# Optimization experiments

Measured on AMD Instinct MI355X. Metric: run time of the kernel, lower is better.

## Reference

```python
import jax, jax.numpy as jnp
import numpy as np

RADIUS, HMIN, HMAX, NSAMPLE = 0.05, -0.02, 0.04, 32
EPS = 1e-5


def setup_inputs() -> dict:
    key = jax.random.key(0)
    ks = jax.random.split(key, 6)
    B, N, C, OUT = 4, 2048, 256, 256
    seed_xyz_graspable = jax.random.uniform(ks[0], (B, N, 3), jnp.float32) * 0.2
    seed_features_graspable = jax.random.normal(ks[1], (B, C, N), jnp.float32)
    vp_rot = jax.random.normal(ks[2], (B, N, 3, 3), jnp.float32)
    W1 = jax.random.normal(ks[3], (OUT, 3 + C), jnp.float32) * 0.02
    W2 = jax.random.normal(ks[4], (OUT, OUT), jnp.float32) * 0.02
    return {
        "seed_xyz_graspable": seed_xyz_graspable,
        "seed_features_graspable": seed_features_graspable,
        "vp_rot": vp_rot,
        "W1": W1, "gamma1": jnp.ones((OUT,), jnp.float32), "beta1": jnp.zeros((OUT,), jnp.float32),
        "W2": W2, "gamma2": jnp.ones((OUT,), jnp.float32), "beta2": jnp.zeros((OUT,), jnp.float32),
    }


def _cylinder_query(xyz, rot):
    # xyz: (B,N,3), rot: (B,N,3,3); new_xyz == xyz.
    B, N, _ = xyz.shape
    d = xyz[:, None, :, :] - xyz[:, :, None, :]                  # (B,P,N,3) offsets to each candidate
    r = jnp.einsum('bpij,bpnj->bpni', rot, d)                    # rotate into cylinder frame (rot @ d)
    mask = (r[..., 1] ** 2 + r[..., 2] ** 2 < RADIUS ** 2) & (r[..., 0] > HMIN) & (r[..., 0] < HMAX)
    order = jnp.arange(N, dtype=jnp.int32)
    keys = jnp.where(mask, order, order + N)                     # in-cylinder points sort first, stable order
    _, idx = jax.lax.top_k(-keys, NSAMPLE)                       # first NSAMPLE indices satisfying the query
    valid = jnp.take_along_axis(mask, idx, axis=-1)
    first = idx[..., :1]
    any_valid = valid[..., :1]
    idx = jnp.where(valid, idx, jnp.where(any_valid, first, 0))  # pad with first hit like the CUDA kernel
    return idx                                                   # (B,P,NSAMPLE) int32


def _group(xyz, features, rot, idx):
    gxyz = jax.vmap(lambda a, i: a[i])(xyz, idx)                 # (B,P,S,3)
    gxyz = (gxyz - xyz[:, :, None, :]) / RADIUS                  # center on query + normalize_xyz
    gxyz = jnp.einsum('bpsj,bpjk->bpsk', gxyz, rot)              # rotate_xyz: grouped_xyz @ rot
    gfeat = jax.vmap(lambda f, i: f[:, i])(features, idx)        # (B,C,P,S)
    return jnp.concatenate([gxyz.transpose(0, 3, 1, 2), gfeat], axis=1)  # (B,3+C,P,S)


def _conv_bn_relu(x, W, gamma, beta):
    y = jnp.einsum('oc,bcps->bops', W, x)                        # 1x1 conv, no bias (bn=True)
    mu = y.mean(axis=(0, 2, 3), keepdims=True)
    var = y.var(axis=(0, 2, 3), keepdims=True)
    y = (y - mu) * jax.lax.rsqrt(var + EPS)
    y = y * gamma[None, :, None, None] + beta[None, :, None, None]
    return jax.nn.relu(y)


def reference(seed_xyz_graspable, seed_features_graspable, vp_rot, W1, gamma1, beta1, W2, gamma2, beta2):
    idx = _cylinder_query(seed_xyz_graspable, vp_rot)
    g = _group(seed_xyz_graspable, seed_features_graspable, vp_rot, idx)
    h = _conv_bn_relu(g, W1, gamma1, beta1)
    h = _conv_bn_relu(h, W2, gamma2, beta2)
    return h.max(axis=3)                                         # maxpool over nsample -> (B,OUT,P)
```

## Files before the change

kernel.cpp:

```cpp
#include <hip/hip_runtime.h>

typedef unsigned short u16;
typedef unsigned int u32;
typedef __attribute__((ext_vector_type(8))) short bf16x8;
typedef __attribute__((ext_vector_type(4))) float f32x4;

#define NPTS 2048
#define CFEAT 256
#define NS 32
#define MTOT 262144
#define NBLK 4096
#define NROW 8192
#define INV_N (1.0f/262144.0f)

__device__ __forceinline__ float bf2f(u16 u) {
    union { u32 i; float f; } v; v.i = ((u32)u) << 16; return v.f;
}
__device__ __forceinline__ u16 f2bf(float f) {
    union { float f; u32 i; } v; v.f = f;
    u32 i = v.i;
    return (u16)((i + 0x7fffu + ((i >> 16) & 1u)) >> 16);
}

__device__ __forceinline__ void gload16(const void* g, void* l) {
    __builtin_amdgcn_global_load_lds((const __attribute__((address_space(1))) void*)g,
                                     (__attribute__((address_space(3))) void*)l, 16, 0, 0);
}

__global__ __launch_bounds__(256) void prep_k(const float* __restrict__ W1, const float* __restrict__ W2,
                                              u16* __restrict__ Wp1, u16* __restrict__ Wp2) {
    int o = blockIdx.x, t = threadIdx.x;
    Wp1[o * 288 + t] = f2bf(W1[o * 259 + 3 + t]);
    if (t < 32) Wp1[o * 288 + 256 + t] = (t < 3) ? f2bf(W1[o * 259 + t]) : (u16)0;
    Wp2[o * 256 + t] = f2bf(W2[o * 256 + t]);
}

__global__ __launch_bounds__(256) void query_k(const float* __restrict__ xyz, const float* __restrict__ rot,
                                               int* __restrict__ idx) {
    int pid = blockIdx.x * 4 + (threadIdx.x >> 6);
    int lane = threadIdx.x & 63;
    int b = pid >> 11, p = pid & 2047;
    const float* xb = xyz + (size_t)b * NPTS * 3;
    float px = xb[p * 3 + 0], py = xb[p * 3 + 1], pz = xb[p * 3 + 2];
    const float* rp = rot + (size_t)pid * 9;
    float r00 = rp[0], r01 = rp[1], r02 = rp[2];
    float r10 = rp[3], r11 = rp[4], r12 = rp[5];
    float r20 = rp[6], r21 = rp[7], r22 = rp[8];
    int cnt = 0, first = 0;
    for (int n0 = 0; n0 < NPTS && cnt < NS; n0 += 64) {
        int n = n0 + lane;
        float dx = __fsub_rn(xb[n * 3 + 0], px);
        float dy = __fsub_rn(xb[n * 3 + 1], py);
        float dz = __fsub_rn(xb[n * 3 + 2], pz);
        float a0 = __fadd_rn(__fadd_rn(__fmul_rn(r00, dx), __fmul_rn(r01, dy)), __fmul_rn(r02, dz));
        float a1 = __fadd_rn(__fadd_rn(__fmul_rn(r10, dx), __fmul_rn(r11, dy)), __fmul_rn(r12, dz));
        float a2 = __fadd_rn(__fadd_rn(__fmul_rn(r20, dx), __fmul_rn(r21, dy)), __fmul_rn(r22, dz));
        float t2 = __fadd_rn(__fmul_rn(a1, a1), __fmul_rn(a2, a2));
        bool valid = (t2 < 0.0025f) && (a0 > -0.02f) && (a0 < 0.04f);
        unsigned long long bal = __ballot(valid);
        if (cnt == 0 && bal) first = n0 + __builtin_ctzll(bal);
        int rank = __builtin_popcountll(bal & ((1ull << lane) - 1ull));
        int slot = cnt + rank;
        if (valid && slot < NS) idx[(size_t)pid * NS + slot] = n;
        cnt += __builtin_popcountll(bal);
    }
    int filled = cnt < NS ? cnt : NS;
    if (lane >= filled && lane < NS) idx[(size_t)pid * NS + lane] = (cnt > 0) ? first : 0;
}

__global__ __launch_bounds__(256) void featT_k(const float* __restrict__ feat, u16* __restrict__ featT) {
    __shared__ float sm[32 * 33];
    int b = blockIdx.z;
    int n0 = blockIdx.x * 32, c0 = blockIdx.y * 32;
    int t = threadIdx.x, x = t & 31, y = t >> 5;
    #pragma unroll
    for (int rr = 0; rr < 4; rr++) {
        int c = c0 + y + rr * 8;
        sm[(y + rr * 8) * 33 + x] = feat[((size_t)(b * CFEAT + c)) * NPTS + n0 + x];
    }
    __syncthreads();
    #pragma unroll
    for (int rr = 0; rr < 4; rr++) {
        int n = n0 + y + rr * 8;
        featT[((size_t)(b * NPTS + n)) * CFEAT + c0 + x] = f2bf(sm[x * 33 + (y + rr * 8)]);
    }
}

__global__ __launch_bounds__(256) void gxyz_k(const float* __restrict__ xyz, const float* __restrict__ rot,
                                              const int* __restrict__ idx, u16* __restrict__ gxyz) {
    int m = blockIdx.x * 256 + threadIdx.x;
    int pid = m >> 5;
    int b = pid >> 11, p = pid & 2047;
    int i = idx[m];
    const float* xb = xyz + (size_t)b * NPTS * 3;
    float dx = (xb[i * 3 + 0] - xb[p * 3 + 0]) * 20.0f;
    float dy = (xb[i * 3 + 1] - xb[p * 3 + 1]) * 20.0f;
    float dz = (xb[i * 3 + 2] - xb[p * 3 + 2]) * 20.0f;
    const float* rp = rot + (size_t)pid * 9;
    float g0 = dx * rp[0] + dy * rp[3] + dz * rp[6];
    float g1 = dx * rp[1] + dy * rp[4] + dz * rp[7];
    float g2 = dx * rp[2] + dy * rp[5] + dz * rp[8];
    uint2 v;
    v.x = (u32)f2bf(g0) | ((u32)f2bf(g1) << 16);
    v.y = (u32)f2bf(g2);
    *(uint2*)(gxyz + (size_t)m * 4) = v;
}

__global__ __launch_bounds__(256) void zero_k(float* __restrict__ p, int n) {
    int i = blockIdx.x * 256 + threadIdx.x;
    if (i < n) p[i] = 0.f;
}

__global__ __launch_bounds__(256) void hist_k(const int* __restrict__ idx, const u16* __restrict__ gxyz,
                                              float* __restrict__ hpart, float* __restrict__ xst64) {
    __shared__ float hist[8192];
    __shared__ float red[9 * 4];
    const int t = threadIdx.x, lane = t & 63, wave = t >> 6;
    const int g = blockIdx.x;
    const int base = g * 4096;
    for (int i = t; i < 8192; i += 256) hist[i] = 0.f;
    __syncthreads();
    float p[9] = {0.f,0.f,0.f,0.f,0.f,0.f,0.f,0.f,0.f};
    for (int u = 0; u < 16; u++) {
        int m = base + u * 256 + t;
        int r = idx[m];
        uint2 v = *(const uint2*)(gxyz + (size_t)m * 4);
        float x0 = bf2f((u16)(v.x & 0xffff));
        float x1 = bf2f((u16)(v.x >> 16));
        float x2 = bf2f((u16)(v.y & 0xffff));
        atomicAdd(hist + r * 4 + 0, 1.f);
        atomicAdd(hist + r * 4 + 1, x0);
        atomicAdd(hist + r * 4 + 2, x1);
        atomicAdd(hist + r * 4 + 3, x2);
        p[0] += x0; p[1] += x1; p[2] += x2;
        p[3] += x0 * x0; p[4] += x0 * x1; p[5] += x0 * x2;
        p[6] += x1 * x1; p[7] += x1 * x2; p[8] += x2 * x2;
    }
    __syncthreads();
    for (int i = t; i < 8192; i += 256) hpart[(size_t)g * 8192 + i] = hist[i];
    #pragma unroll
    for (int k = 0; k < 9; k++) {
        float s = p[k];
        #pragma unroll
        for (int o = 1; o < 64; o <<= 1) s += __shfl_xor(s, o);
        if (lane == 0) red[k * 4 + wave] = s;
    }
    __syncthreads();
    if (t < 9) xst64[g * 9 + t] = red[t * 4 + 0] + red[t * 4 + 1] + red[t * 4 + 2] + red[t * 4 + 3];
}

__global__ __launch_bounds__(256) void merge_k(const float* __restrict__ hpart, float* __restrict__ cntx) {
    int i = blockIdx.x * 256 + threadIdx.x;
    int b = i >> 13;
    int off = i & 8191;
    float s = 0.f;
    #pragma unroll
    for (int sg = 0; sg < 16; sg++) s += hpart[(size_t)(b * 16 + sg) * 8192 + off];
    cntx[i] = s;
}

__global__ __launch_bounds__(256) void zgemm_k(const u16* __restrict__ featT, const u16* __restrict__ Wp1,
                                               const float* __restrict__ cntx,
                                               float* __restrict__ Sacc, float* __restrict__ Qacc,
                                               float* __restrict__ Xacc) {
    __shared__ __attribute__((aligned(16))) u16 As[64 * 32];
    __shared__ __attribute__((aligned(16))) u16 Bs[256 * 32];
    const int tid = threadIdx.x;
    const int lane = tid & 63, wave = tid >> 6;
    const int quad = lane >> 4, tl = lane & 15;
    const int m0 = blockIdx.x * 64;
    const int srow = tid >> 2, sc16 = tid & 3;
    const int abase = (m0 + srow) * CFEAT + sc16 * 8;

    f32x4 acc[4][4];
    #pragma unroll
    for (int i = 0; i < 4; i++)
        #pragma unroll
        for (int j = 0; j < 4; j++) acc[i][j] = (f32x4){0.f, 0.f, 0.f, 0.f};

    for (int ks = 0; ks < 8; ks++) {
        const int k0 = ks * 32;
        __syncthreads();
        gload16(featT + abase + k0, As + tid * 8);
        #pragma unroll
        for (int q = 0; q < 4; q++)
            gload16(Wp1 + (srow + q * 64) * 288 + k0 + sc16 * 8, Bs + q * 2048 + tid * 8);
        __syncthreads();
        bf16x8 af[4], bv[4];
        #pragma unroll
        for (int i = 0; i < 4; i++) af[i] = *(const bf16x8*)(As + (i * 16 + tl) * 32 + quad * 8);
        #pragma unroll
        for (int j = 0; j < 4; j++) bv[j] = *(const bf16x8*)(Bs + (wave * 64 + j * 16 + tl) * 32 + quad * 8);
        #pragma unroll
        for (int i = 0; i < 4; i++)
            #pragma unroll
            for (int j = 0; j < 4; j++)
                acc[i][j] = __builtin_amdgcn_mfma_f32_16x16x32_bf16(af[i], bv[j], acc[i][j], 0, 0, 0);
    }

    #pragma unroll
    for (int j = 0; j < 4; j++) {
        int col = wave * 64 + j * 16 + tl;
        float wx0 = bf2f(Wp1[col * 288 + 256]);
        float wx1 = bf2f(Wp1[col * 288 + 257]);
        float wx2 = bf2f(Wp1[col * 288 + 258]);
        float S = 0.f, Q = 0.f, X = 0.f;
        #pragma unroll
        for (int i = 0; i < 4; i++)
            #pragma unroll
            for (int rr = 0; rr < 4; rr++) {
                int row = i * 16 + quad * 4 + rr;
                float4 cx = *(const float4*)(cntx + (size_t)(m0 + row) * 4);
                float z = acc[i][j][rr];
                S += cx.x * z;
                Q += cx.x * z * z;
                X += z * (wx0 * cx.y + wx1 * cx.z + wx2 * cx.w);
            }
        S += __shfl_xor(S, 16); S += __shfl_xor(S, 32);
        Q += __shfl_xor(Q, 16); Q += __shfl_xor(Q, 32);
        X += __shfl_xor(X, 16); X += __shfl_xor(X, 32);
        if (quad == 0) {
            atomicAdd(Sacc + col, S);
            atomicAdd(Qacc + col, Q);
            atomicAdd(Xacc + col, X);
        }
    }
}

__global__ __launch_bounds__(256) void ab1_k(const float* __restrict__ Sacc, const float* __restrict__ Qacc,
                                             const float* __restrict__ Xacc, const float* __restrict__ xst64,
                                             const u16* __restrict__ Wp1,
                                             const float* __restrict__ gamma, const float* __restrict__ beta,
                                             float* __restrict__ ab) {
    int c = threadIdx.x;
    float xs[9] = {0.f,0.f,0.f,0.f,0.f,0.f,0.f,0.f,0.f};
    for (int g = 0; g < 64; g++)
        #pragma unroll
        for (int k = 0; k < 9; k++) xs[k] += xst64[g * 9 + k];
    float wx0 = bf2f(Wp1[c * 288 + 256]);
    float wx1 = bf2f(Wp1[c * 288 + 257]);
    float wx2 = bf2f(Wp1[c * 288 + 258]);
    float S = Sacc[c] + wx0 * xs[0] + wx1 * xs[1] + wx2 * xs[2];
    float qxx = wx0 * wx0 * xs[3] + wx1 * wx1 * xs[6] + wx2 * wx2 * xs[8]
              + 2.f * (wx0 * wx1 * xs[4] + wx0 * wx2 * xs[5] + wx1 * wx2 * xs[7]);
    float Q = Qacc[c] + 2.f * Xacc[c] + qxx;
    float mu = S * INV_N;
    float var = Q * INV_N - mu * mu;
    float a = gamma[c] * rsqrtf(var + 1e-5f);
    ab[c] = a;
    ab[256 + c] = beta[c] - mu * a;
}

template <int FULL>
__global__ __launch_bounds__(256) void fused_k(
    const u16* __restrict__ featT, const u16* __restrict__ gxyz, const int* __restrict__ idx,
    const u16* __restrict__ Wp1, const u16* __restrict__ Wp2, const float* __restrict__ ab1,
    float* __restrict__ psum, float* __restrict__ psq,
    float* __restrict__ ymax, float* __restrict__ ymin)
{
    __shared__ __attribute__((aligned(16))) u16 As[64 * 32];
    __shared__ __attribute__((aligned(16))) u16 Bs[256 * 32];
    __shared__ __attribute__((aligned(16))) u16 y1s[FULL ? 64 * 264 : 16];
    __shared__ int rowbase_s[64];

    const int tid = threadIdx.x;
    const int lane = tid & 63, wave = tid >> 6;
    const int quad = lane >> 4, tl = lane & 15;
    const int bx = blockIdx.x;
    const int m0 = bx * 64;

    if (tid < 64) {
        int m = m0 + tid;
        int gi = idx[m];
        int b = m >> 16;
        rowbase_s[tid] = (b * NPTS + gi) * CFEAT;
    }
    __syncthreads();
    const int srow = tid >> 2, sc16 = tid & 3;
    const int abase = rowbase_s[srow] + sc16 * 8;

    f32x4 acc[4][4];
    #pragma unroll
    for (int i = 0; i < 4; i++)
        #pragma unroll
        for (int j = 0; j < 4; j++) acc[i][j] = (f32x4){0.f, 0.f, 0.f, 0.f};

    auto mfma_tile = [&](f32x4 (&ac)[4][4], const u16* a_lds, int a_stride) {
        bf16x8 af[4], bv[4];
        #pragma unroll
        for (int i = 0; i < 4; i++) af[i] = *(const bf16x8*)(a_lds + (i * 16 + tl) * a_stride + quad * 8);
        #pragma unroll
        for (int j = 0; j < 4; j++) bv[j] = *(const bf16x8*)(Bs + (wave * 64 + j * 16 + tl) * 32 + quad * 8);
        #pragma unroll
        for (int i = 0; i < 4; i++)
            #pragma unroll
            for (int j = 0; j < 4; j++)
                ac[i][j] = __builtin_amdgcn_mfma_f32_16x16x32_bf16(af[i], bv[j], ac[i][j], 0, 0, 0);
    };

    for (int ks = 0; ks < 8; ks++) {
        const int k0 = ks * 32;
        __syncthreads();
        gload16(featT + abase + k0, As + tid * 8);
        #pragma unroll
        for (int q = 0; q < 4; q++)
            gload16(Wp1 + (srow + q * 64) * 288 + k0 + sc16 * 8, Bs + q * 2048 + tid * 8);
        __syncthreads();
        mfma_tile(acc, As, 32);
    }
    {
        __syncthreads();
        uint4 va = make_uint4(0, 0, 0, 0);
        if (sc16 == 0) {
            uint2 g2 = *(const uint2*)(gxyz + (size_t)(m0 + srow) * 4);
            va.x = g2.x; va.y = g2.y;
        }
        *(uint4*)(As + srow * 32 + sc16 * 8) = va;
        #pragma unroll
        for (int q = 0; q < 4; q++)
            gload16(Wp1 + (srow + q * 64) * 288 + 256 + sc16 * 8, Bs + q * 2048 + tid * 8);
        __syncthreads();
        mfma_tile(acc, As, 32);
    }

    if (!FULL) {
        #pragma unroll
        for (int j = 0; j < 4; j++) {
            float s = 0.f, q2 = 0.f;
            #pragma unroll
            for (int i = 0; i < 4; i++) {
                s += acc[i][j][0] + acc[i][j][1] + acc[i][j][2] + acc[i][j][3];
                q2 += acc[i][j][0]*acc[i][j][0] + acc[i][j][1]*acc[i][j][1]
                    + acc[i][j][2]*acc[i][j][2] + acc[i][j][3]*acc[i][j][3];
            }
            s += __shfl_xor(s, 16); s += __shfl_xor(s, 32);
            q2 += __shfl_xor(q2, 16); q2 += __shfl_xor(q2, 32);
            if (quad == 0) {
                int col = wave * 64 + j * 16 + tl;
                psum[(size_t)bx * 256 + col] = s;
                psq[(size_t)bx * 256 + col] = q2;
            }
        }
        return;
    }

    #pragma unroll
    for (int j = 0; j < 4; j++) {
        int col = wave * 64 + j * 16 + tl;
        float a = ab1[col], bb = ab1[256 + col];
        #pragma unroll
        for (int i = 0; i < 4; i++)
            #pragma unroll
            for (int r = 0; r < 4; r++) {
                float v = fmaxf(fmaf(acc[i][j][r], a, bb), 0.f);
                y1s[(i * 16 + quad * 4 + r) * 264 + col] = f2bf(v);
            }
    }

    f32x4 acc2[4][4];
    #pragma unroll
    for (int i = 0; i < 4; i++)
        #pragma unroll
        for (int j = 0; j < 4; j++) acc2[i][j] = (f32x4){0.f, 0.f, 0.f, 0.f};
    for (int ks = 0; ks < 8; ks++) {
        const int k0 = ks * 32;
        __syncthreads();
        #pragma unroll
        for (int q = 0; q < 4; q++)
            gload16(Wp2 + (srow + q * 64) * 256 + k0 + sc16 * 8, Bs + q * 2048 + tid * 8);
        __syncthreads();
        mfma_tile(acc2, y1s + k0, 264);
    }

    #pragma unroll
    for (int j = 0; j < 4; j++) {
        int col = wave * 64 + j * 16 + tl;
        float s = 0.f, q2 = 0.f;
        float mx0 = -3.0e38f, mn0 = 3.0e38f, mx1 = -3.0e38f, mn1 = 3.0e38f;
        #pragma unroll
        for (int i = 0; i < 4; i++)
            #pragma unroll
            for (int r = 0; r < 4; r++) {
                float v = acc2[i][j][r];
                s += v; q2 += v * v;
                if (i < 2) { mx0 = fmaxf(mx0, v); mn0 = fminf(mn0, v); }
                else       { mx1 = fmaxf(mx1, v); mn1 = fminf(mn1, v); }
            }
        s += __shfl_xor(s, 16); s += __shfl_xor(s, 32);
        q2 += __shfl_xor(q2, 16); q2 += __shfl_xor(q2, 32);
        mx0 = fmaxf(mx0, __shfl_xor(mx0, 16)); mx0 = fmaxf(mx0, __shfl_xor(mx0, 32));
        mn0 = fminf(mn0, __shfl_xor(mn0, 16)); mn0 = fminf(mn0, __shfl_xor(mn0, 32));
        mx1 = fmaxf(mx1, __shfl_xor(mx1, 16)); mx1 = fmaxf(mx1, __shfl_xor(mx1, 32));
        mn1 = fminf(mn1, __shfl_xor(mn1, 16)); mn1 = fminf(mn1, __shfl_xor(mn1, 32));
        if (quad == 0) {
            psum[(size_t)bx * 256 + col] = s;
            psq[(size_t)bx * 256 + col] = q2;
            size_t p0 = (size_t)(bx * 2) * 256 + col;
            size_t p1 = (size_t)(bx * 2 + 1) * 256 + col;
            ymax[p0] = mx0; ymin[p0] = mn0;
            ymax[p1] = mx1; ymin[p1] = mn1;
        }
    }
}

__global__ __launch_bounds__(256) void reduce1_k(const float* __restrict__ psum, const float* __restrict__ psq,
                                                 float* __restrict__ ps2, float* __restrict__ pq2) {
    int j = blockIdx.x, t = threadIdx.x;
    float s = 0.f, q = 0.f;
    #pragma unroll 4
    for (int kk = 0; kk < 64; kk++) {
        size_t r = (size_t)(j * 64 + kk) * 256 + t;
        s += psum[r]; q += psq[r];
    }
    ps2[j * 256 + t] = s;
    pq2[j * 256 + t] = q;
}

__global__ __launch_bounds__(256) void reduce2_k(const float* __restrict__ ps2, const float* __restrict__ pq2,
                                                 const float* __restrict__ gamma, const float* __restrict__ beta,
                                                 float* __restrict__ ab) {
    int c = threadIdx.x;
    float S = 0.f, Q = 0.f;
    for (int j = 0; j < 64; j++) {
        S += ps2[j * 256 + c];
        Q += pq2[j * 256 + c];
    }
    float mu = S * INV_N;
    float var = Q * INV_N - mu * mu;
    float a = gamma[c] * rsqrtf(var + 1e-5f);
    ab[c] = a;
    ab[256 + c] = beta[c] - mu * a;
}

__global__ __launch_bounds__(256) void final_k(const float* __restrict__ ymax, const float* __restrict__ ymin,
                                               const float* __restrict__ ab, float* __restrict__ out) {
    __shared__ float sm[32 * 33];
    int b = blockIdx.z;
    int n0 = blockIdx.x * 32, o0 = blockIdx.y * 32;
    int t = threadIdx.x, x = t & 31, y = t >> 5;
    #pragma unroll
    for (int rr = 0; rr < 4; rr++) {
        int n = n0 + y + rr * 8;
        int o = o0 + x;
        float a = ab[o], bb = ab[256 + o];
        size_t p = (size_t)(b * NPTS + n) * 256 + o;
        float v = (a >= 0.f) ? ymax[p] : ymin[p];
        sm[(y + rr * 8) * 33 + x] = fmaxf(fmaf(v, a, bb), 0.f);
    }
    __syncthreads();
    #pragma unroll
    for (int rr = 0; rr < 4; rr++)
        out[((size_t)(b * 256 + o0 + y + rr * 8)) * NPTS + n0 + x] = sm[x * 33 + (y + rr * 8)];
}

extern "C" void kernel_launch(void* const* d_in, const int* in_sizes, int n_in,
                              void* d_out, int out_size, void* d_ws, size_t ws_size,
                              hipStream_t stream) {
    const float* xyz    = (const float*)d_in[0];
    const float* feat   = (const float*)d_in[1];
    const float* rot    = (const float*)d_in[2];
    const float* W1     = (const float*)d_in[3];
    const float* gamma1 = (const float*)d_in[4];
    const float* beta1  = (const float*)d_in[5];
    const float* W2     = (const float*)d_in[6];
    const float* gamma2 = (const float*)d_in[7];
    const float* beta2  = (const float*)d_in[8];
    float* out = (float*)d_out;

    char* ws = (char*)d_ws;
    u16*   featT = (u16*)(ws + 0);
    int*   idxp  = (int*)(ws + 4194304);
    u16*   gxyz  = (u16*)(ws + 5242880);
    u16*   Wp1   = (u16*)(ws + 7340032);
    u16*   Wp2   = (u16*)(ws + 7487488);
    float* ab1   = (float*)(ws + 7618560);
    float* ab2   = (float*)(ws + 7620608);
    float* cntx  = (float*)(ws + 7622656);
    float* Sacc  = (float*)(ws + 7753728);
    float* Qacc  = (float*)(ws + 7754752);
    float* Xacc  = (float*)(ws + 7755776);
    float* xst64 = (float*)(ws + 7756800);
    float* hpart = (float*)(ws + 7760896);
    float* psum  = (float*)(ws + 9858048);
    float* psq   = (float*)(ws + 14052352);
    float* ymax  = (float*)(ws + 18246656);
    float* ymin  = (float*)(ws + 26635264);
    const size_t NEED = 35023872ull;

    float* r1s = (float*)(ws + 26635264);
    float* r1q = r1s + 16384;
    float* r2s = (float*)(ws + 5242880);
    float* r2q = r2s + 16384;

    prep_k<<<256, 256, 0, stream>>>(W1, W2, Wp1, Wp2);
    query_k<<<2048, 256, 0, stream>>>(xyz, rot, idxp);
    featT_k<<<dim3(64, 8, 4), 256, 0, stream>>>(feat, featT);
    gxyz_k<<<1024, 256, 0, stream>>>(xyz, rot, idxp, gxyz);

    if (ws_size >= NEED) {
        zero_k<<<3, 256, 0, stream>>>(Sacc, 768);
        hist_k<<<64, 256, 0, stream>>>(idxp, gxyz, hpart, xst64);
        merge_k<<<128, 256, 0, stream>>>(hpart, cntx);
        zgemm_k<<<NROW / 64, 256, 0, stream>>>(featT, Wp1, cntx, Sacc, Qacc, Xacc);
        ab1_k<<<1, 256, 0, stream>>>(Sacc, Qacc, Xacc, xst64, Wp1, gamma1, beta1, ab1);
        fused_k<1><<<NBLK, 256, 0, stream>>>(featT, gxyz, idxp, Wp1, Wp2, ab1, psum, psq, ymax, ymin);
        reduce1_k<<<64, 256, 0, stream>>>(psum, psq, r2s, r2q);
        reduce2_k<<<1, 256, 0, stream>>>(r2s, r2q, gamma2, beta2, ab2);
    } else {
        fused_k<0><<<NBLK, 256, 0, stream>>>(featT, gxyz, idxp, Wp1, Wp2, ab1, psum, psq, ymax, ymin);
        reduce1_k<<<64, 256, 0, stream>>>(psum, psq, r1s, r1q);
        reduce2_k<<<1, 256, 0, stream>>>(r1s, r1q, gamma1, beta1, ab1);
        fused_k<1><<<NBLK, 256, 0, stream>>>(featT, gxyz, idxp, Wp1, Wp2, ab1, psum, psq, ymax, ymin);
        reduce1_k<<<64, 256, 0, stream>>>(psum, psq, r2s, r2q);
        reduce2_k<<<1, 256, 0, stream>>>(r2s, r2q, gamma2, beta2, ab2);
    }
    final_k<<<dim3(64, 8, 4), 256, 0, stream>>>(ymax, ymin, ab2, out);
}
```

Baseline: 283.4 us.

## Halve y1 LDS buffer, fuse histogram merge into zgemm, raise fused occupancy

The fused kernel's column-to-wave mapping is interleaved so each wave owns columns j*64+wave*16. This lets the layer-1 activation tile in LDS hold only 128 columns at a time. The second half is written after the first four K steps of the second GEMM, which shrinks LDS and lets launch_bounds request 3 blocks per SM. The separate merge kernel is removed because zgemm now sums the 16 histogram partials into shared memory itself, and the zero kernel is replaced by hipMemsetAsync. Risks are an extra barrier inside the GEMM2 loop and register pressure from the occupancy hint.

```diff
diff --git a/kernel.cpp b/kernel.cpp
--- a/kernel.cpp
+++ b/kernel.cpp
@@ -106,11 +106,6 @@
     *(uint2*)(gxyz + (size_t)m * 4) = v;
 }
 
-__global__ __launch_bounds__(256) void zero_k(float* __restrict__ p, int n) {
-    int i = blockIdx.x * 256 + threadIdx.x;
-    if (i < n) p[i] = 0.f;
-}
-
 __global__ __launch_bounds__(256) void hist_k(const int* __restrict__ idx, const u16* __restrict__ gxyz,
                                               float* __restrict__ hpart, float* __restrict__ xst64) {
     __shared__ float hist[8192];
@@ -149,22 +144,13 @@
     if (t < 9) xst64[g * 9 + t] = red[t * 4 + 0] + red[t * 4 + 1] + red[t * 4 + 2] + red[t * 4 + 3];
 }
 
-__global__ __launch_bounds__(256) void merge_k(const float* __restrict__ hpart, float* __restrict__ cntx) {
-    int i = blockIdx.x * 256 + threadIdx.x;
-    int b = i >> 13;
-    int off = i & 8191;
-    float s = 0.f;
-    #pragma unroll
-    for (int sg = 0; sg < 16; sg++) s += hpart[(size_t)(b * 16 + sg) * 8192 + off];
-    cntx[i] = s;
-}
-
 __global__ __launch_bounds__(256) void zgemm_k(const u16* __restrict__ featT, const u16* __restrict__ Wp1,
-                                               const float* __restrict__ cntx,
+                                               const float* __restrict__ hpart,
                                                float* __restrict__ Sacc, float* __restrict__ Qacc,
                                                float* __restrict__ Xacc) {
     __shared__ __attribute__((aligned(16))) u16 As[64 * 32];
     __shared__ __attribute__((aligned(16))) u16 Bs[256 * 32];
+    __shared__ float cxs[64 * 4];
     const int tid = threadIdx.x;
     const int lane = tid & 63, wave = tid >> 6;
     const int quad = lane >> 4, tl = lane & 15;
@@ -172,6 +158,17 @@
     const int srow = tid >> 2, sc16 = tid & 3;
     const int abase = (m0 + srow) * CFEAT + sc16 * 8;
 
+    {
+        const int b = m0 >> 11;
+        const int rl0 = m0 & 2047;
+        int row = tid >> 2, c = tid & 3;
+        float s = 0.f;
+        #pragma unroll
+        for (int sg = 0; sg < 16; sg++)
+            s += hpart[(size_t)(b * 16 + sg) * 8192 + (rl0 + row) * 4 + c];
+        cxs[tid] = s;
+    }
+
     f32x4 acc[4][4];
     #pragma unroll
     for (int i = 0; i < 4; i++)
@@ -210,7 +207,7 @@
             #pragma unroll
             for (int rr = 0; rr < 4; rr++) {
                 int row = i * 16 + quad * 4 + rr;
-                float4 cx = *(const float4*)(cntx + (size_t)(m0 + row) * 4);
+                float4 cx = *(const float4*)(cxs + row * 4);
                 float z = acc[i][j][rr];
                 S += cx.x * z;
                 Q += cx.x * z * z;
@@ -252,7 +249,7 @@
 }
 
 template <int FULL>
-__global__ __launch_bounds__(256) void fused_k(
+__global__ __launch_bounds__(256, 3) void fused_k(
     const u16* __restrict__ featT, const u16* __restrict__ gxyz, const int* __restrict__ idx,
     const u16* __restrict__ Wp1, const u16* __restrict__ Wp2, const float* __restrict__ ab1,
     float* __restrict__ psum, float* __restrict__ psq,
@@ -260,7 +257,7 @@
 {
     __shared__ __attribute__((aligned(16))) u16 As[64 * 32];
     __shared__ __attribute__((aligned(16))) u16 Bs[256 * 32];
-    __shared__ __attribute__((aligned(16))) u16 y1s[FULL ? 64 * 264 : 16];
+    __shared__ __attribute__((aligned(16))) u16 y1s[FULL ? 64 * 136 : 16];
     __shared__ int rowbase_s[64];
 
     const int tid = threadIdx.x;
@@ -290,7 +287,7 @@
         #pragma unroll
         for (int i = 0; i < 4; i++) af[i] = *(const bf16x8*)(a_lds + (i * 16 + tl) * a_stride + quad * 8);
         #pragma unroll
-        for (int j = 0; j < 4; j++) bv[j] = *(const bf16x8*)(Bs + (wave * 64 + j * 16 + tl) * 32 + quad * 8);
+        for (int j = 0; j < 4; j++) bv[j] = *(const bf16x8*)(Bs + (j * 64 + wave * 16 + tl) * 32 + quad * 8);
         #pragma unroll
         for (int i = 0; i < 4; i++)
             #pragma unroll
@@ -336,7 +333,7 @@
             s += __shfl_xor(s, 16); s += __shfl_xor(s, 32);
             q2 += __shfl_xor(q2, 16); q2 += __shfl_xor(q2, 32);
             if (quad == 0) {
-                int col = wave * 64 + j * 16 + tl;
+                int col = j * 64 + wave * 16 + tl;
                 psum[(size_t)bx * 256 + col] = s;
                 psq[(size_t)bx * 256 + col] = q2;
             }
@@ -345,15 +342,15 @@
     }
 
     #pragma unroll
-    for (int j = 0; j < 4; j++) {
-        int col = wave * 64 + j * 16 + tl;
+    for (int j = 0; j < 2; j++) {
+        int col = j * 64 + wave * 16 + tl;
         float a = ab1[col], bb = ab1[256 + col];
         #pragma unroll
         for (int i = 0; i < 4; i++)
             #pragma unroll
             for (int r = 0; r < 4; r++) {
                 float v = fmaxf(fmaf(acc[i][j][r], a, bb), 0.f);
-                y1s[(i * 16 + quad * 4 + r) * 264 + col] = f2bf(v);
+                y1s[(i * 16 + quad * 4 + r) * 136 + col] = f2bf(v);
             }
     }
 
@@ -363,18 +360,35 @@
         #pragma unroll
         for (int j = 0; j < 4; j++) acc2[i][j] = (f32x4){0.f, 0.f, 0.f, 0.f};
     for (int ks = 0; ks < 8; ks++) {
+        if (ks == 4) {
+            __syncthreads();
+            #pragma unroll
+            for (int j = 2; j < 4; j++) {
+                int col = j * 64 + wave * 16 + tl;
+                int lc = col - 128;
+                float a = ab1[col], bb = ab1[256 + col];
+                #pragma unroll
+                for (int i = 0; i < 4; i++)
+                    #pragma unroll
+                    for (int r = 0; r < 4; r++) {
+                        float v = fmaxf(fmaf(acc[i][j][r], a, bb), 0.f);
+                        y1s[(i * 16 + quad * 4 + r) * 136 + lc] = f2bf(v);
+                    }
+            }
+        }
         const int k0 = ks * 32;
+        const int kl = k0 & 127;
         __syncthreads();
         #pragma unroll
         for (int q = 0; q < 4; q++)
             gload16(Wp2 + (srow + q * 64) * 256 + k0 + sc16 * 8, Bs + q * 2048 + tid * 8);
         __syncthreads();
-        mfma_tile(acc2, y1s + k0, 264);
+        mfma_tile(acc2, y1s + kl, 136);
     }
 
     #pragma unroll
     for (int j = 0; j < 4; j++) {
-        int col = wave * 64 + j * 16 + tl;
+        int col = j * 64 + wave * 16 + tl;
         float s = 0.f, q2 = 0.f;
         float mx0 = -3.0e38f, mn0 = 3.0e38f, mx1 = -3.0e38f, mn1 = 3.0e38f;
         #pragma unroll
@@ -475,7 +489,6 @@
     u16*   Wp2   = (u16*)(ws + 7487488);
     float* ab1   = (float*)(ws + 7618560);
     float* ab2   = (float*)(ws + 7620608);
-    float* cntx  = (float*)(ws + 7622656);
     float* Sacc  = (float*)(ws + 7753728);
     float* Qacc  = (float*)(ws + 7754752);
     float* Xacc  = (float*)(ws + 7755776);
@@ -498,10 +511,9 @@
     gxyz_k<<<1024, 256, 0, stream>>>(xyz, rot, idxp, gxyz);
 
     if (ws_size >= NEED) {
-        zero_k<<<3, 256, 0, stream>>>(Sacc, 768);
+        hipMemsetAsync(Sacc, 0, 3 * 1024, stream);
         hist_k<<<64, 256, 0, stream>>>(idxp, gxyz, hpart, xst64);
-        merge_k<<<128, 256, 0, stream>>>(hpart, cntx);
-        zgemm_k<<<NROW / 64, 256, 0, stream>>>(featT, Wp1, cntx, Sacc, Qacc, Xacc);
+        zgemm_k<<<NROW / 64, 256, 0, stream>>>(featT, Wp1, hpart, Sacc, Qacc, Xacc);
         ab1_k<<<1, 256, 0, stream>>>(Sacc, Qacc, Xacc, xst64, Wp1, gamma1, beta1, ab1);
         fused_k<1><<<NBLK, 256, 0, stream>>>(featT, gxyz, idxp, Wp1, Wp2, ab1, psum, psq, ymax, ymin);
         reduce1_k<<<64, 256, 0, stream>>>(psum, psq, r2s, r2q);
```

After: 267.4 us. 1.06x faster.
